# Kernel tuning notes

Hardware: AMD Instinct MI355X
Metric: run time of the kernel (lower is better)

Reference implementation:

```python
import jax, jax.numpy as jnp
import numpy as np

B, T, C = 4, 2048, 1024   # batch, seq_len, n_embd
H, D = 16, 64             # num heads, head dim (H*D == C)


def setup_inputs() -> dict:
    key = jax.random.key(0)
    ks = jax.random.split(key, 6)
    scale = 0.02
    x = jax.random.normal(ks[0], (B, T, C), dtype=jnp.float32)
    Wq = jax.random.normal(ks[1], (H, C, D), dtype=jnp.float32) * scale
    Wk = jax.random.normal(ks[2], (H, C, D), dtype=jnp.float32) * scale
    Wv = jax.random.normal(ks[3], (H, C, D), dtype=jnp.float32) * scale
    Wp = jax.random.normal(ks[4], (C, C), dtype=jnp.float32) * scale
    bp = jnp.zeros((C,), dtype=jnp.float32)
    return {"x": x, "Wq": Wq, "Wk": Wk, "Wv": Wv, "Wp": Wp, "bp": bp}


def reference(x, Wq, Wk, Wv, Wp, bp):
    # Batched per-head projections (equivalent to the per-head nn.Linear loop)
    q = jnp.einsum('btc,hcd->bhtd', x, Wq)
    k = jnp.einsum('btc,hcd->bhtd', x, Wk)
    v = jnp.einsum('btc,hcd->bhtd', x, Wv)
    # NOTE: original code scales by C**-0.5 where C = n_embd (not head dim)
    scores = jnp.einsum('bhtd,bhsd->bhts', q, k) * (C ** -0.5)
    causal = jnp.tril(jnp.ones((T, T), dtype=bool))  # [T, T]
    scores = jnp.where(causal, scores, -jnp.inf)
    att = jax.nn.softmax(scores, axis=-1)            # [B, H, T, T]
    out = jnp.einsum('bhts,bhsd->bhtd', att, v)      # [B, H, T, D]
    # concat heads (order matches torch.cat over head list) then output proj
    out = out.transpose(0, 2, 1, 3).reshape(B, T, H * D)
    return out @ Wp + bp
```

## Files before the change

kernel.cpp:

```cpp
#include <hip/hip_runtime.h>
#include <hip/hip_bf16.h>


#define B_ 4
#define T_ 2048
#define C_ 1024
#define H_ 16
#define D_ 64
#define M_ (B_*T_)

typedef unsigned short u16;
typedef unsigned short ushort8 __attribute__((ext_vector_type(8)));
typedef unsigned int uint4v __attribute__((ext_vector_type(4)));
typedef int int2v __attribute__((ext_vector_type(2)));
typedef __attribute__((ext_vector_type(8))) short bf16x8;
typedef __attribute__((ext_vector_type(4))) float f32x4;
typedef __attribute__((ext_vector_type(16))) float f32x16;

__device__ __forceinline__ u16 f2bf(float f) {
    __hip_bfloat16 h = __float2bfloat16(f);
    return *reinterpret_cast<u16*>(&h);
}
__device__ __forceinline__ unsigned pkt(float lo, float hi2) {
    return __builtin_amdgcn_perm(__float_as_uint(hi2), __float_as_uint(lo), 0x07060302u);
}
__device__ __forceinline__ void gload_lds16(const void* g, void* lds) {
    __builtin_amdgcn_global_load_lds((const __attribute__((address_space(1))) unsigned int*)g,
                                     (__attribute__((address_space(3))) unsigned int*)lds, 16, 0, 0);
}
__device__ __forceinline__ int swzf(int r) { return (r ^ (r >> 2)) & 3; }

__global__ __launch_bounds__(256) void cast_x(const float* __restrict__ in, u16* __restrict__ out) {
    int i = (blockIdx.x * 256 + threadIdx.x) * 8;
    float4 a = *reinterpret_cast<const float4*>(in + i);
    float4 b = *reinterpret_cast<const float4*>(in + i + 4);
    ushort8 o;
    o[0]=f2bf(a.x); o[1]=f2bf(a.y); o[2]=f2bf(a.z); o[3]=f2bf(a.w);
    o[4]=f2bf(b.x); o[5]=f2bf(b.y); o[6]=f2bf(b.z); o[7]=f2bf(b.w);
    *reinterpret_cast<ushort8*>(out + i) = o;
}

__device__ __forceinline__ void ttile64(const float* __restrict__ in, int ldin,
                                        u16* __restrict__ out, int ldout, float scale) {
    __shared__ float t[64][65];
    const int tid = threadIdx.x;
    {
        int c = tid & 63, rr = tid >> 6;
        #pragma unroll
        for (int i = 0; i < 16; ++i) {
            int r = i * 4 + rr;
            t[r][c] = in[(size_t)r * ldin + c];
        }
    }
    __syncthreads();
    {
        int r2 = tid & 63, cg = tid >> 6;
        #pragma unroll
        for (int i = 0; i < 16; ++i) {
            int cc = i * 4 + cg;
            out[(size_t)cc * ldout + r2] = f2bf(t[r2][cc] * scale);
        }
    }
}

__global__ __launch_bounds__(256) void tw_qkv(const float* __restrict__ Wq, const float* __restrict__ Wk,
                                              const float* __restrict__ Wv, u16* __restrict__ Wt) {
    const int z = blockIdx.y;
    const int which = z >> 4, h = z & 15;
    const float* W = (which == 0 ? Wq : which == 1 ? Wk : Wv) + (size_t)h * C_ * D_;
    const int r0 = blockIdx.x * 64;
    const float scale = (which == 0) ? 0.03125f * 1.4426950408889634f : 1.f;
    ttile64(W + (size_t)r0 * D_, D_, Wt + (size_t)(which * 16 + h) * 64 * C_ + r0, C_, scale);
}

__global__ __launch_bounds__(256) void tw_p(const float* __restrict__ Wp, u16* __restrict__ Wpt) {
    const int r0 = blockIdx.x * 64, c0 = blockIdx.y * 64;
    ttile64(Wp + (size_t)r0 * C_ + c0, C_, Wpt + (size_t)c0 * C_ + r0, C_, 1.f);
}

__global__ __launch_bounds__(256) void tv(const u16* __restrict__ v, u16* __restrict__ vT) {
    __shared__ u16 t[64][72];
    const int tid = threadIdx.x;
    const int t0 = blockIdx.x * 64, bh = blockIdx.y;
    const u16* src = v + ((size_t)bh * T_ + t0) * D_;
    #pragma unroll
    for (int it = 0; it < 2; ++it) {
        int idx = it * 256 + tid;
        int r = idx >> 3, c8 = (idx & 7) * 8;
        *reinterpret_cast<ushort8*>(&t[r][c8]) =
            *reinterpret_cast<const ushort8*>(src + (size_t)r * D_ + c8);
    }
    __syncthreads();
    #pragma unroll
    for (int it = 0; it < 2; ++it) {
        int idx = it * 256 + tid;
        int d = idx >> 3, c8 = (idx & 7) * 8;
        ushort8 w;
        #pragma unroll
        for (int i = 0; i < 8; ++i) w[i] = t[c8 + i][d];
        *reinterpret_cast<ushort8*>(vT + ((size_t)bh * D_ + d) * T_ + t0 + c8) = w;
    }
}

__device__ __forceinline__ void gemm_core(const u16* __restrict__ A, const u16* __restrict__ Bt,
                                          int m0, int n0, u16* lds, f32x4 (&acc)[4][4]) {
    const int tid = threadIdx.x;
    const int wid = tid >> 6, lane = tid & 63;
    const int l16 = lane & 15, lq = lane >> 4;
    const int wr = wid >> 1, wc = wid & 1;

    const int rA0 = tid >> 2, rA1 = 128 + (tid >> 2), rB = tid >> 2, gd = tid & 3;
    const u16* sA0 = A  + (size_t)(m0 + rA0) * C_ + ((gd ^ swzf(rA0)) * 8);
    const u16* sA1 = A  + (size_t)(m0 + rA1) * C_ + ((gd ^ swzf(rA1)) * 8);
    const u16* sB0 = Bt + (size_t)(n0 + rB)  * C_ + ((gd ^ swzf(rB))  * 8);

    const char* lb = reinterpret_cast<const char*>(lds);
    const int gcol = ((lq ^ ((l16 ^ (l16 >> 2)) & 3)) & 3) * 16;
    int aoff[4], boff[4];
    #pragma unroll
    for (int i = 0; i < 4; ++i) {
        aoff[i] = (wr * 64 + i * 16 + l16) * 64 + gcol;
        boff[i] = 16384 + (wc * 64 + i * 16 + l16) * 64 + gcol;
    }

#define STG3(BU16)                                                                  \
    {                                                                               \
        gload_lds16(sA0, lds + (BU16) + tid * 8);                                   \
        gload_lds16(sA1, lds + (BU16) + 4096 + tid * 8);                            \
        gload_lds16(sB0, lds + (BU16) + 8192 + tid * 8);                            \
        sA0 += 32; sA1 += 32; sB0 += 32;                                            \
    }

    STG3(0);
    STG3(12288);

    #pragma unroll
    for (int t = 0; t < 32; ++t) {
        if (t + 2 < 32) {
            STG3(((t + 2) % 3) * 12288);
            asm volatile("s_waitcnt vmcnt(6)" ::: "memory");
        } else if (t + 1 < 32) {
            asm volatile("s_waitcnt vmcnt(3)" ::: "memory");
        } else {
            asm volatile("s_waitcnt vmcnt(0)" ::: "memory");
        }
        __builtin_amdgcn_sched_barrier(0);
        __builtin_amdgcn_s_barrier();
        __builtin_amdgcn_sched_barrier(0);

        const char* lbuf = lb + (t % 3) * 24576;
        __builtin_amdgcn_s_setprio(1);
        bf16x8 bfr[4];
        #pragma unroll
        for (int nt = 0; nt < 4; ++nt)
            bfr[nt] = *reinterpret_cast<const bf16x8*>(lbuf + boff[nt]);
        #pragma unroll
        for (int mt = 0; mt < 4; ++mt) {
            bf16x8 af = *reinterpret_cast<const bf16x8*>(lbuf + aoff[mt]);
            #pragma unroll
            for (int nt = 0; nt < 4; ++nt)
                acc[mt][nt] = __builtin_amdgcn_mfma_f32_16x16x32_bf16(af, bfr[nt], acc[mt][nt], 0, 0, 0);
        }
        __builtin_amdgcn_s_setprio(0);
        __builtin_amdgcn_sched_barrier(0);
        __builtin_amdgcn_s_barrier();
        __builtin_amdgcn_sched_barrier(0);
    }
#undef STG3
}

__global__ __launch_bounds__(512, 4) void qkv_gemm(const u16* __restrict__ xb, const u16* __restrict__ Wt,
                                                   u16* __restrict__ q, u16* __restrict__ k,
                                                   u16* __restrict__ v) {
    __shared__ u16 lds[3 * 12288];
    f32x4 acc[4][4];
    #pragma unroll
    for (int i = 0; i < 4; ++i)
        #pragma unroll
        for (int j = 0; j < 4; ++j) { acc[i][j][0]=0.f; acc[i][j][1]=0.f; acc[i][j][2]=0.f; acc[i][j][3]=0.f; }
    const int m0 = blockIdx.x * 256, n0 = blockIdx.y * 128;
    gemm_core(xb, Wt, m0, n0, lds, acc);

    const int tid = threadIdx.x, wid = tid >> 6, lane = tid & 63;
    const int l16 = lane & 15, lq = lane >> 4;
    const int wr = wid >> 1, wc = wid & 1;
    #pragma unroll
    for (int mt = 0; mt < 4; ++mt) {
        #pragma unroll
        for (int j = 0; j < 4; ++j) {
            int m = m0 + wr * 64 + mt * 16 + lq * 4 + j;
            int b = m >> 11, t = m & (T_ - 1);
            #pragma unroll
            for (int nt = 0; nt < 4; ++nt) {
                int n = n0 + wc * 64 + nt * 16 + l16;
                int which = n >> 10, h = (n >> 6) & 15, d = n & 63;
                u16* dst = (which == 0 ? q : which == 1 ? k : v);
                dst[((size_t)(b * H_ + h) * T_ + t) * D_ + d] = f2bf(acc[mt][nt][j]);
            }
        }
    }
}

__global__ __launch_bounds__(512, 4) void out_gemm(const u16* __restrict__ ob, const u16* __restrict__ Wpt,
                                                   const float* __restrict__ bp, float* __restrict__ out) {
    __shared__ u16 lds[3 * 12288];
    f32x4 acc[4][4];
    #pragma unroll
    for (int i = 0; i < 4; ++i)
        #pragma unroll
        for (int j = 0; j < 4; ++j) { acc[i][j][0]=0.f; acc[i][j][1]=0.f; acc[i][j][2]=0.f; acc[i][j][3]=0.f; }
    const int m0 = blockIdx.x * 256, n0 = blockIdx.y * 128;
    gemm_core(ob, Wpt, m0, n0, lds, acc);

    const int tid = threadIdx.x, wid = tid >> 6, lane = tid & 63;
    const int l16 = lane & 15, lq = lane >> 4;
    const int wr = wid >> 1, wc = wid & 1;
    #pragma unroll
    for (int mt = 0; mt < 4; ++mt) {
        #pragma unroll
        for (int j = 0; j < 4; ++j) {
            int m = m0 + wr * 64 + mt * 16 + lq * 4 + j;
            #pragma unroll
            for (int nt = 0; nt < 4; ++nt) {
                int n = n0 + wc * 64 + nt * 16 + l16;
                out[(size_t)m * C_ + n] = acc[mt][nt][j] + bp[n];
            }
        }
    }
}

template<int CUR>
__device__ __forceinline__ void attn_tile(const char* const (&pf)[4], const bf16x8 (&qf)[4],
                                          const f32x16& z16, float& lrun,
                                          f32x16& oacc0, f32x16& oacc1,
                                          bool isdiag, int relq, int hi) {
    f32x16 st0, st1;
    __builtin_amdgcn_s_setprio(1);
    {
        bf16x8 ka0 = *reinterpret_cast<const bf16x8*>(pf[0] + CUR * 32768);
        bf16x8 ka1 = *reinterpret_cast<const bf16x8*>(pf[0] + CUR * 32768 + 4096);
        st0 = __builtin_amdgcn_mfma_f32_32x32x16_bf16(ka0, qf[0], z16, 0, 0, 0);
        st1 = __builtin_amdgcn_mfma_f32_32x32x16_bf16(ka1, qf[0], z16, 0, 0, 0);
    }
    #pragma unroll
    for (int kc = 1; kc < 4; ++kc) {
        bf16x8 ka0 = *reinterpret_cast<const bf16x8*>(pf[kc] + CUR * 32768);
        bf16x8 ka1 = *reinterpret_cast<const bf16x8*>(pf[kc] + CUR * 32768 + 4096);
        st0 = __builtin_amdgcn_mfma_f32_32x32x16_bf16(ka0, qf[kc], st0, 0, 0, 0);
        st1 = __builtin_amdgcn_mfma_f32_32x32x16_bf16(ka1, qf[kc], st1, 0, 0, 0);
    }
    __builtin_amdgcn_s_setprio(0);

    if (isdiag) {
        #pragma unroll
        for (int rr = 0; rr < 16; ++rr) {
            int sl = (rr & 3) + 8 * (rr >> 2) + 4 * hi;
            if (sl > relq)      st0[rr] = -INFINITY;
            if (sl + 32 > relq) st1[rr] = -INFINITY;
        }
    }

    float rsum = 0.f;
    #pragma unroll
    for (int rr = 0; rr < 16; ++rr) {
        st0[rr] = __builtin_amdgcn_exp2f(st0[rr]);
        st1[rr] = __builtin_amdgcn_exp2f(st1[rr]);
        rsum += st0[rr] + st1[rr];
    }
    rsum += __shfl_xor(rsum, 32);
    lrun += rsum;

    bf16x8 pa0, pa1, pa2, pa3;
#if __has_builtin(__builtin_amdgcn_permlane32_swap)
#define MK_PA(PA, SV, RB)                                                          \
    {                                                                              \
        int X0 = (int)pkt(SV[RB + 0], SV[RB + 1]);                                 \
        int X1 = (int)pkt(SV[RB + 2], SV[RB + 3]);                                 \
        int Y0 = (int)pkt(SV[RB + 4], SV[RB + 5]);                                 \
        int Y1 = (int)pkt(SV[RB + 6], SV[RB + 7]);                                 \
        int2v r0 = __builtin_amdgcn_permlane32_swap(X0, Y0, false, false);         \
        int2v r1 = __builtin_amdgcn_permlane32_swap(X1, Y1, false, false);         \
        uint4v w; w[0] = (unsigned)r0[0]; w[1] = (unsigned)r1[0];                  \
        w[2] = (unsigned)r0[1]; w[3] = (unsigned)r1[1];                            \
        PA = __builtin_bit_cast(bf16x8, w);                                        \
    }
#else
#define MK_PA(PA, SV, RB)                                                          \
    {                                                                              \
        unsigned X0 = pkt(SV[RB + 0], SV[RB + 1]);                                 \
        unsigned X1 = pkt(SV[RB + 2], SV[RB + 3]);                                 \
        unsigned Y0 = pkt(SV[RB + 4], SV[RB + 5]);                                 \
        unsigned sX0 = __shfl_xor(X0, 32), sY0 = __shfl_xor(Y0, 32);               \
        unsigned Y1 = pkt(SV[RB + 6], SV[RB + 7]);                                 \
        unsigned sX1 = __shfl_xor(X1, 32), sY1 = __shfl_xor(Y1, 32);               \
        uint4v w;                                                                  \
        w[0] = hi ? sY0 : X0; w[1] = hi ? sY1 : X1;                                \
        w[2] = hi ? Y0 : sX0; w[3] = hi ? Y1 : sX1;                                \
        PA = __builtin_bit_cast(bf16x8, w);                                        \
    }
#endif
    MK_PA(pa0, st0, 0); MK_PA(pa1, st0, 8); MK_PA(pa2, st1, 0); MK_PA(pa3, st1, 8);
#undef MK_PA

    __builtin_amdgcn_s_setprio(1);
#define PV_STEP(SCJ, PAV)                                                          \
    {                                                                              \
        bf16x8 va0 = *reinterpret_cast<const bf16x8*>(pf[SCJ] + CUR * 32768 + 16384);        \
        bf16x8 va1 = *reinterpret_cast<const bf16x8*>(pf[SCJ] + CUR * 32768 + 16384 + 4096); \
        oacc0 = __builtin_amdgcn_mfma_f32_32x32x16_bf16(va0, PAV, oacc0, 0, 0, 0); \
        oacc1 = __builtin_amdgcn_mfma_f32_32x32x16_bf16(va1, PAV, oacc1, 0, 0, 0); \
    }
    PV_STEP(0, pa0) PV_STEP(1, pa1) PV_STEP(2, pa2) PV_STEP(3, pa3)
#undef PV_STEP
    __builtin_amdgcn_s_setprio(0);
}

__global__ __launch_bounds__(512, 4) void attn_mfma(const u16* __restrict__ q,
                                                    const u16* __restrict__ k,
                                                    const u16* __restrict__ vT,
                                                    u16* __restrict__ o) {
    __shared__ u16 smem[32768];

    const int tid  = threadIdx.x;
    const int wid  = tid >> 6;
    const int lane = tid & 63;
    const int l31  = lane & 31;
    const int hi   = lane >> 5;

    const int lin = blockIdx.x;
    const int r   = lin & 255;
    const int f   = lin >> 8;
    const int bh  = r & 63;
    const int e   = r >> 6;
    const int qb  = f ? (7 - e) : e;

    const int q0 = qb * 256;
    const size_t base = (size_t)bh * T_ * D_;
    const u16* kp  = k  + base;
    const u16* vtp = vT + (size_t)bh * D_ * T_;
    const int qglob = q0 + wid * 32 + l31;

    bf16x8 qf[4];
    {
        const u16* qp = q + base + (size_t)qglob * D_;
        #pragma unroll
        for (int kc = 0; kc < 4; ++kc)
            qf[kc] = *reinterpret_cast<const bf16x8*>(qp + kc * 16 + hi * 8);
    }

    const int rw = tid >> 3;
    const int cg = (tid & 7) ^ (rw & 7);
    const u16* gK = kp  + (size_t)rw * D_ + cg * 8;
    const u16* gV = vtp + (size_t)rw * T_ + cg * 8;

    u16* sbase = &smem[0];
    u16* dK = sbase + tid * 8;
    u16* dV = sbase + 8192 + tid * 8;

    const char* pf[4];
    #pragma unroll
    for (int j = 0; j < 4; ++j)
        pf[j] = reinterpret_cast<const char*>(sbase) + l31 * 128 + (((j * 2 + hi) ^ (l31 & 7)) << 4);

    float lrun = 0.f;
    f32x16 oacc0, oacc1, z16;
    #pragma unroll
    for (int rr = 0; rr < 16; ++rr) { oacc0[rr] = 0.f; oacc1[rr] = 0.f; z16[rr] = 0.f; }

    const int ntile  = 4 * qb + 4;
    const int diag_t = 4 * qb + (wid >> 1);
    const int relq   = 32 * (wid & 1) + l31;

#define STG(BUFU16)                                                                \
    {                                                                              \
        gload_lds16(gK, dK + (BUFU16)); gload_lds16(gV, dV + (BUFU16));            \
        gK += 64 * D_; gV += 64;                                                   \
    }

    STG(0);
    __syncthreads();

    for (int tt = 0; tt < ntile; tt += 2) {
        if (tt + 1 < ntile) STG(16384);
        if (tt <= diag_t)
            attn_tile<0>(pf, qf, z16, lrun, oacc0, oacc1, tt == diag_t, relq, hi);
        __syncthreads();
        if (tt + 2 < ntile) STG(0);
        if (tt + 1 <= diag_t)
            attn_tile<1>(pf, qf, z16, lrun, oacc0, oacc1, tt + 1 == diag_t, relq, hi);
        __syncthreads();
    }
#undef STG

    float linv = 1.f / lrun;
    float* ot = reinterpret_cast<float*>(sbase) + wid * 2048;
    #pragma unroll
    for (int rr = 0; rr < 16; ++rr) {
        int d0v = (rr & 3) + 8 * (rr >> 2) + 4 * hi;
        int d1v = d0v + 32;
        ot[l31 * 64 + (((d0v >> 2) ^ (l31 & 7)) << 2) + (d0v & 3)] = oacc0[rr] * linv;
        ot[l31 * 64 + (((d1v >> 2) ^ (l31 & 7)) << 2) + (d1v & 3)] = oacc1[rr] * linv;
    }

    const int b = bh >> 4, h = bh & 15;
    const int qrow = lane >> 1;
    const int d0 = (lane & 1) * 32;
    u16 tmp[32];
    #pragma unroll
    for (int i = 0; i < 8; ++i) {
        int g = ((d0 >> 2) + i) ^ (qrow & 7);
        float4 fv = *reinterpret_cast<const float4*>(&ot[qrow * 64 + (g << 2)]);
        tmp[i * 4 + 0] = f2bf(fv.x); tmp[i * 4 + 1] = f2bf(fv.y);
        tmp[i * 4 + 2] = f2bf(fv.z); tmp[i * 4 + 3] = f2bf(fv.w);
    }
    u16* orow = o + ((size_t)b * T_ + q0 + wid * 32 + qrow) * C_ + h * 64 + d0;
    #pragma unroll
    for (int j = 0; j < 4; ++j)
        *reinterpret_cast<ushort8*>(orow + j * 8) = *reinterpret_cast<ushort8*>(&tmp[j * 8]);
}

extern "C" void kernel_launch(void* const* d_in, const int* in_sizes, int n_in,
                              void* d_out, int out_size, void* d_ws, size_t ws_size,
                              hipStream_t stream) {
    const float* x  = (const float*)d_in[0];
    const float* Wq = (const float*)d_in[1];
    const float* Wk = (const float*)d_in[2];
    const float* Wv = (const float*)d_in[3];
    const float* Wp = (const float*)d_in[4];
    const float* bp = (const float*)d_in[5];
    float* out = (float*)d_out;

    const size_t E = (size_t)M_ * C_;
    u16* xb  = (u16*)d_ws;
    u16* qb  = xb  + E;
    u16* kb  = qb  + E;
    u16* vb  = kb  + E;
    u16* obf = vb  + E;
    u16* Wt  = obf + E;
    u16* Wpt = Wt  + (size_t)3072 * 1024;
    u16* vTb = xb;

    cast_x<<<(E / 2048), 256, 0, stream>>>(x, xb);
    tw_qkv<<<dim3(16, 48), 256, 0, stream>>>(Wq, Wk, Wv, Wt);
    tw_p<<<dim3(16, 16), 256, 0, stream>>>(Wp, Wpt);

    qkv_gemm<<<dim3(M_ / 256, 3072 / 128), 512, 0, stream>>>(xb, Wt, qb, kb, vb);

    tv<<<dim3(T_ / 64, B_ * H_), 256, 0, stream>>>(vb, vTb);

    attn_mfma<<<dim3(512), 512, 0, stream>>>(qb, kb, vTb, obf);

    out_gemm<<<dim3(M_ / 256, C_ / 128), 512, 0, stream>>>(obf, Wpt, bp, out);
}
```

Measured before the change: 149.8 us.

## Restructure projection GEMMs to 4-wave blocks with 32x32 MFMA and double buffering

Rewrites the shared GEMM core used by the QKV and output projections. Blocks drop from 8 waves to 4, and each wave now computes a 128x64 tile using 32x32x16 bf16 MFMAs instead of a 64x64 tile with 16x16x32 MFMAs. The LDS pipeline goes from triple to double buffering, with the next stage issued after the trailing barrier. The intent is to raise MFMA work per LDS read and cut per-wave overhead. The cost is more accumulator registers, lower occupancy and a shallower prefetch pipeline that can expose memory latency.

```diff
diff --git a/kernel.cpp b/kernel.cpp
--- a/kernel.cpp
+++ b/kernel.cpp
@@ -14,7 +14,6 @@
 typedef unsigned int uint4v __attribute__((ext_vector_type(4)));
 typedef int int2v __attribute__((ext_vector_type(2)));
 typedef __attribute__((ext_vector_type(8))) short bf16x8;
-typedef __attribute__((ext_vector_type(4))) float f32x4;
 typedef __attribute__((ext_vector_type(16))) float f32x16;
 
 __device__ __forceinline__ u16 f2bf(float f) {
@@ -28,7 +27,7 @@
     __builtin_amdgcn_global_load_lds((const __attribute__((address_space(1))) unsigned int*)g,
                                      (__attribute__((address_space(3))) unsigned int*)lds, 16, 0, 0);
 }
-__device__ __forceinline__ int swzf(int r) { return (r ^ (r >> 2)) & 3; }
+__device__ __forceinline__ int swz4(int r) { return (r ^ (r >> 2)) & 3; }
 
 __global__ __launch_bounds__(256) void cast_x(const float* __restrict__ in, u16* __restrict__ out) {
     int i = (blockIdx.x * 256 + threadIdx.x) * 8;
@@ -102,128 +101,142 @@
     }
 }
 
-__device__ __forceinline__ void gemm_core(const u16* __restrict__ A, const u16* __restrict__ Bt,
-                                          int m0, int n0, u16* lds, f32x4 (&acc)[4][4]) {
+__device__ __forceinline__ void gemm_core3(const u16* __restrict__ A, const u16* __restrict__ Bt,
+                                           int m0, int n0, u16* lds, f32x16 (&acc)[4][2]) {
     const int tid = threadIdx.x;
     const int wid = tid >> 6, lane = tid & 63;
-    const int l16 = lane & 15, lq = lane >> 4;
+    const int l31 = lane & 31, hi = lane >> 5;
     const int wr = wid >> 1, wc = wid & 1;
 
-    const int rA0 = tid >> 2, rA1 = 128 + (tid >> 2), rB = tid >> 2, gd = tid & 3;
-    const u16* sA0 = A  + (size_t)(m0 + rA0) * C_ + ((gd ^ swzf(rA0)) * 8);
-    const u16* sA1 = A  + (size_t)(m0 + rA1) * C_ + ((gd ^ swzf(rA1)) * 8);
-    const u16* sB0 = Bt + (size_t)(n0 + rB)  * C_ + ((gd ^ swzf(rB))  * 8);
+    const u16* src[6];
+    #pragma unroll
+    for (int it = 0; it < 6; ++it) {
+        int slot = it * 256 + tid;
+        int row, g;
+        const u16* base;
+        if (it < 4) { row = slot >> 2; g = slot & 3; base = A + (size_t)(m0 + row) * C_; }
+        else        { int s2 = slot - 1024; row = s2 >> 2; g = s2 & 3; base = Bt + (size_t)(n0 + row) * C_; }
+        src[it] = base + ((g ^ swz4(row)) * 8);
+    }
 
     const char* lb = reinterpret_cast<const char*>(lds);
-    const int gcol = ((lq ^ ((l16 ^ (l16 >> 2)) & 3)) & 3) * 16;
-    int aoff[4], boff[4];
-    #pragma unroll
-    for (int i = 0; i < 4; ++i) {
-        aoff[i] = (wr * 64 + i * 16 + l16) * 64 + gcol;
-        boff[i] = 16384 + (wc * 64 + i * 16 + l16) * 64 + gcol;
-    }
-
-#define STG3(BU16)                                                                  \
+    int aoff[2][4], boff[2][2];
+    #pragma unroll
+    for (int kk = 0; kk < 2; ++kk) {
+        #pragma unroll
+        for (int mt = 0; mt < 4; ++mt) {
+            int row = wr * 128 + mt * 32 + l31;
+            aoff[kk][mt] = row * 64 + (((kk * 2 + hi) ^ swz4(row)) & 3) * 16;
+        }
+        #pragma unroll
+        for (int nt = 0; nt < 2; ++nt) {
+            int row = wc * 64 + nt * 32 + l31;
+            boff[kk][nt] = 16384 + row * 64 + (((kk * 2 + hi) ^ swz4(row)) & 3) * 16;
+        }
+    }
+
+#define STG(BU16)                                                                   \
     {                                                                               \
-        gload_lds16(sA0, lds + (BU16) + tid * 8);                                   \
-        gload_lds16(sA1, lds + (BU16) + 4096 + tid * 8);                            \
-        gload_lds16(sB0, lds + (BU16) + 8192 + tid * 8);                            \
-        sA0 += 32; sA1 += 32; sB0 += 32;                                            \
-    }
-
-    STG3(0);
-    STG3(12288);
+        _Pragma("unroll")                                                           \
+        for (int it = 0; it < 6; ++it) {                                            \
+            gload_lds16(src[it], lds + (BU16) + (it * 256 + tid) * 8);              \
+            src[it] += 32;                                                          \
+        }                                                                           \
+    }
+
+    STG(0);
+    STG(12288);
 
     #pragma unroll
     for (int t = 0; t < 32; ++t) {
-        if (t + 2 < 32) {
-            STG3(((t + 2) % 3) * 12288);
-            asm volatile("s_waitcnt vmcnt(6)" ::: "memory");
-        } else if (t + 1 < 32) {
-            asm volatile("s_waitcnt vmcnt(3)" ::: "memory");
-        } else {
-            asm volatile("s_waitcnt vmcnt(0)" ::: "memory");
-        }
+        if (t < 31) { asm volatile("s_waitcnt vmcnt(6)" ::: "memory"); }
+        else        { asm volatile("s_waitcnt vmcnt(0)" ::: "memory"); }
         __builtin_amdgcn_sched_barrier(0);
         __builtin_amdgcn_s_barrier();
         __builtin_amdgcn_sched_barrier(0);
 
-        const char* lbuf = lb + (t % 3) * 24576;
+        const char* lbuf = lb + (t & 1) * 24576;
         __builtin_amdgcn_s_setprio(1);
-        bf16x8 bfr[4];
-        #pragma unroll
-        for (int nt = 0; nt < 4; ++nt)
-            bfr[nt] = *reinterpret_cast<const bf16x8*>(lbuf + boff[nt]);
-        #pragma unroll
-        for (int mt = 0; mt < 4; ++mt) {
-            bf16x8 af = *reinterpret_cast<const bf16x8*>(lbuf + aoff[mt]);
+        #pragma unroll
+        for (int kk = 0; kk < 2; ++kk) {
+            bf16x8 bf0 = *reinterpret_cast<const bf16x8*>(lbuf + boff[kk][0]);
+            bf16x8 bf1 = *reinterpret_cast<const bf16x8*>(lbuf + boff[kk][1]);
             #pragma unroll
-            for (int nt = 0; nt < 4; ++nt)
-                acc[mt][nt] = __builtin_amdgcn_mfma_f32_16x16x32_bf16(af, bfr[nt], acc[mt][nt], 0, 0, 0);
+            for (int mt = 0; mt < 4; ++mt) {
+                bf16x8 af = *reinterpret_cast<const bf16x8*>(lbuf + aoff[kk][mt]);
+                acc[mt][0] = __builtin_amdgcn_mfma_f32_32x32x16_bf16(af, bf0, acc[mt][0], 0, 0, 0);
+                acc[mt][1] = __builtin_amdgcn_mfma_f32_32x32x16_bf16(af, bf1, acc[mt][1], 0, 0, 0);
+            }
         }
         __builtin_amdgcn_s_setprio(0);
         __builtin_amdgcn_sched_barrier(0);
         __builtin_amdgcn_s_barrier();
         __builtin_amdgcn_sched_barrier(0);
-    }
-#undef STG3
-}
-
-__global__ __launch_bounds__(512, 4) void qkv_gemm(const u16* __restrict__ xb, const u16* __restrict__ Wt,
+        if (t + 2 < 32) STG((t & 1) * 12288);
+    }
+#undef STG
+}
+
+__global__ __launch_bounds__(256, 2) void qkv_gemm(const u16* __restrict__ xb, const u16* __restrict__ Wt,
                                                    u16* __restrict__ q, u16* __restrict__ k,
                                                    u16* __restrict__ v) {
-    __shared__ u16 lds[3 * 12288];
-    f32x4 acc[4][4];
+    __shared__ u16 lds[2 * 12288];
+    f32x16 acc[4][2];
     #pragma unroll
     for (int i = 0; i < 4; ++i)
         #pragma unroll
-        for (int j = 0; j < 4; ++j) { acc[i][j][0]=0.f; acc[i][j][1]=0.f; acc[i][j][2]=0.f; acc[i][j][3]=0.f; }
+        for (int j = 0; j < 2; ++j)
+            #pragma unroll
+            for (int r = 0; r < 16; ++r) acc[i][j][r] = 0.f;
     const int m0 = blockIdx.x * 256, n0 = blockIdx.y * 128;
-    gemm_core(xb, Wt, m0, n0, lds, acc);
+    gemm_core3(xb, Wt, m0, n0, lds, acc);
 
     const int tid = threadIdx.x, wid = tid >> 6, lane = tid & 63;
-    const int l16 = lane & 15, lq = lane >> 4;
+    const int l31 = lane & 31, hi = lane >> 5;
     const int wr = wid >> 1, wc = wid & 1;
     #pragma unroll
     for (int mt = 0; mt < 4; ++mt) {
         #pragma unroll
-        for (int j = 0; j < 4; ++j) {
-            int m = m0 + wr * 64 + mt * 16 + lq * 4 + j;
-            int b = m >> 11, t = m & (T_ - 1);
+        for (int nt = 0; nt < 2; ++nt) {
+            int n = n0 + wc * 64 + nt * 32 + l31;
+            int which = n >> 10, h = (n >> 6) & 15, d = n & 63;
+            u16* dst = (which == 0 ? q : which == 1 ? k : v);
             #pragma unroll
-            for (int nt = 0; nt < 4; ++nt) {
-                int n = n0 + wc * 64 + nt * 16 + l16;
-                int which = n >> 10, h = (n >> 6) & 15, d = n & 63;
-                u16* dst = (which == 0 ? q : which == 1 ? k : v);
-                dst[((size_t)(b * H_ + h) * T_ + t) * D_ + d] = f2bf(acc[mt][nt][j]);
+            for (int r = 0; r < 16; ++r) {
+                int m = m0 + wr * 128 + mt * 32 + (r & 3) + 8 * (r >> 2) + 4 * hi;
+                int b = m >> 11, t = m & (T_ - 1);
+                dst[((size_t)(b * H_ + h) * T_ + t) * D_ + d] = f2bf(acc[mt][nt][r]);
             }
         }
     }
 }
 
-__global__ __launch_bounds__(512, 4) void out_gemm(const u16* __restrict__ ob, const u16* __restrict__ Wpt,
+__global__ __launch_bounds__(256, 2) void out_gemm(const u16* __restrict__ ob, const u16* __restrict__ Wpt,
                                                    const float* __restrict__ bp, float* __restrict__ out) {
-    __shared__ u16 lds[3 * 12288];
-    f32x4 acc[4][4];
+    __shared__ u16 lds[2 * 12288];
+    f32x16 acc[4][2];
     #pragma unroll
     for (int i = 0; i < 4; ++i)
         #pragma unroll
-        for (int j = 0; j < 4; ++j) { acc[i][j][0]=0.f; acc[i][j][1]=0.f; acc[i][j][2]=0.f; acc[i][j][3]=0.f; }
+        for (int j = 0; j < 2; ++j)
+            #pragma unroll
+            for (int r = 0; r < 16; ++r) acc[i][j][r] = 0.f;
     const int m0 = blockIdx.x * 256, n0 = blockIdx.y * 128;
-    gemm_core(ob, Wpt, m0, n0, lds, acc);
+    gemm_core3(ob, Wpt, m0, n0, lds, acc);
 
     const int tid = threadIdx.x, wid = tid >> 6, lane = tid & 63;
-    const int l16 = lane & 15, lq = lane >> 4;
+    const int l31 = lane & 31, hi = lane >> 5;
     const int wr = wid >> 1, wc = wid & 1;
     #pragma unroll
     for (int mt = 0; mt < 4; ++mt) {
         #pragma unroll
-        for (int j = 0; j < 4; ++j) {
-            int m = m0 + wr * 64 + mt * 16 + lq * 4 + j;
+        for (int nt = 0; nt < 2; ++nt) {
+            int n = n0 + wc * 64 + nt * 32 + l31;
+            float bv = bp[n];
             #pragma unroll
-            for (int nt = 0; nt < 4; ++nt) {
-                int n = n0 + wc * 64 + nt * 16 + l16;
-                out[(size_t)m * C_ + n] = acc[mt][nt][j] + bp[n];
+            for (int r = 0; r < 16; ++r) {
+                int m = m0 + wr * 128 + mt * 32 + (r & 3) + 8 * (r >> 2) + 4 * hi;
+                out[(size_t)m * C_ + n] = acc[mt][nt][r] + bv;
             }
         }
     }
@@ -444,11 +457,11 @@
     tw_qkv<<<dim3(16, 48), 256, 0, stream>>>(Wq, Wk, Wv, Wt);
     tw_p<<<dim3(16, 16), 256, 0, stream>>>(Wp, Wpt);
 
-    qkv_gemm<<<dim3(M_ / 256, 3072 / 128), 512, 0, stream>>>(xb, Wt, qb, kb, vb);
+    qkv_gemm<<<dim3(M_ / 256, 3072 / 128), 256, 0, stream>>>(xb, Wt, qb, kb, vb);
 
     tv<<<dim3(T_ / 64, B_ * H_), 256, 0, stream>>>(vb, vTb);
 
     attn_mfma<<<dim3(512), 512, 0, stream>>>(qb, kb, vTb, obf);
 
-    out_gemm<<<dim3(M_ / 256, C_ / 128), 512, 0, stream>>>(obf, Wpt, bp, out);
-}
+    out_gemm<<<dim3(M_ / 256, C_ / 128), 256, 0, stream>>>(obf, Wpt, bp, out);
+}
```

Measured after the change: 152.1 us. No clear change (+1.5%).
